# Kernel optimization log

Measured on AMD Instinct MI355X. Metric: run time of the kernel, lower is better.

## Reference

```python
import jax, jax.numpy as jnp
import numpy as np

B, H, W, C_IN, F = 4, 64, 64, 128, 256


def setup_inputs() -> dict:
    key = jax.random.key(0)
    ks = jax.random.split(key, 6)
    return {
        "inputs": jax.random.normal(ks[0], (B, H, W, C_IN), dtype=jnp.float32),
        "W_proj": jax.random.normal(ks[1], (C_IN, F), dtype=jnp.float32) * 0.02,
        "b_proj": jnp.zeros((F,), dtype=jnp.float32),
        "W_q": jax.random.normal(ks[2], (F, F), dtype=jnp.float32) * 0.02,
        "b_q": jnp.zeros((F,), dtype=jnp.float32),
        "W_k": jax.random.normal(ks[3], (F, F), dtype=jnp.float32) * 0.02,
        "b_k": jnp.zeros((F,), dtype=jnp.float32),
        "W_v": jax.random.normal(ks[4], (F, F), dtype=jnp.float32) * 0.02,
        "b_v": jnp.zeros((F,), dtype=jnp.float32),
        "gamma": jax.random.uniform(ks[5], (1,), dtype=jnp.float32),
    }


def reference(inputs, W_proj, b_proj, W_q, b_q, W_k, b_k, W_v, b_v, gamma):
    # 1x1 conv projection (C_in -> filters) since input channels != filters
    x = jnp.einsum("bhwc,cf->bhwf", inputs, W_proj) + b_proj  # [B,H,W,F]
    q = jnp.einsum("bhwf,fg->bhwg", x, W_q) + b_q
    k = jnp.einsum("bhwf,fg->bhwg", x, W_k) + b_k
    v = jnp.einsum("bhwf,fg->bhwg", x, W_v) + b_v
    b, h, w, f = x.shape
    n = h * w
    qr = q.reshape(b, n, f)
    kr = k.reshape(b, n, f)
    vr = v.reshape(b, n, f)
    attn = jax.nn.softmax(jnp.einsum("bnf,bmf->bnm", qr, kr), axis=-1)  # [B,N,N]
    context = jnp.einsum("bnm,bmf->bnf", attn, vr).reshape(b, h, w, f)
    return gamma * context + x
```

## Files before the change

kernel.cpp:

```cpp
#include <hip/hip_runtime.h>
#include <hip/hip_bf16.h>
#include <stdint.h>

typedef __attribute__((ext_vector_type(8))) short short8;
typedef __attribute__((ext_vector_type(4))) float floatx4;
typedef __attribute__((ext_vector_type(16))) float floatx16;
typedef __attribute__((ext_vector_type(2))) long longx2;

#define DEVI __device__ __forceinline__
#define MFMA16(a, b, c) __builtin_amdgcn_mfma_f32_16x16x32_bf16((a), (b), (c), 0, 0, 0)
#define MFMA32(a, b, c) __builtin_amdgcn_mfma_f32_32x32x16_fp8_fp8((a), (b), (c), 0, 0, 0)

typedef __attribute__((address_space(3))) unsigned int lds_u32;
typedef __attribute__((address_space(1))) const unsigned int glb_u32;
#define GLOAD_LDS16(g, l) __builtin_amdgcn_global_load_lds((glb_u32*)(g), (lds_u32*)(l), 16, 0, 0)

DEVI unsigned short f2bf(float x) {
    union { float f; unsigned int u; } v; v.f = x;
    unsigned int r = v.u + 0x7FFFu + ((v.u >> 16) & 1u);
    return (unsigned short)(r >> 16);
}
DEVI float bf2f(unsigned short h) {
    union { unsigned int u; float f; } v; v.u = ((unsigned int)h) << 16;
    return v.f;
}
DEVI unsigned char f2fp8(float x) {
    int c = __builtin_amdgcn_cvt_pk_fp8_f32(x, x, 0, false);
    return (unsigned char)(c & 0xFF);
}

__global__ __launch_bounds__(256) void prep_weights(
    const float* __restrict__ Wp, const float* __restrict__ Wq,
    const float* __restrict__ Wk, const float* __restrict__ Wv,
    unsigned short* __restrict__ Tp, unsigned short* __restrict__ Tq,
    unsigned short* __restrict__ Tk, unsigned short* __restrict__ Tv)
{
    int idx = blockIdx.x * blockDim.x + threadIdx.x;
    if (idx < 32768) {
        int k = idx >> 8, n = idx & 255;
        Tp[n * 128 + k] = f2bf(Wp[idx]);
    } else {
        int r = idx - 32768;
        int m = r >> 16, i = r & 65535;
        const float* W   = (m == 0) ? Wq : (m == 1) ? Wk : Wv;
        unsigned short* T = (m == 0) ? Tq : (m == 1) ? Tk : Tv;
        int k = i >> 8, n = i & 255;
        T[n * 256 + k] = f2bf(W[i]);
    }
}


__global__ __launch_bounds__(256) void gemm_bias(
    const float* __restrict__ A,
    const unsigned short* __restrict__ Wt,
    const float* __restrict__ bias,
    unsigned short* __restrict__ Cb,
    int N)
{
    __shared__ __align__(16) unsigned short As[64][136];
    __shared__ __align__(16) unsigned short Bs[64][136];
    const int tid  = threadIdx.x;
    const int w    = tid >> 6;
    const int lane = tid & 63;
    const int quad = lane >> 4;
    const int l15  = lane & 15;
    const int m0 = blockIdx.x * 64;
    const int n0 = blockIdx.y * 64;

    floatx4 acc[4];
    #pragma unroll
    for (int t = 0; t < 4; ++t) acc[t] = (floatx4)0.0f;

    #pragma unroll
    for (int it = 0; it < 8; ++it) {
        int idx = tid + it * 256;
        int r = idx >> 5, c4 = idx & 31;
        float4 v = *(const float4*)&A[(size_t)(m0 + r) * 128 + c4 * 4];
        ushort4 o;
        o.x = f2bf(v.x); o.y = f2bf(v.y); o.z = f2bf(v.z); o.w = f2bf(v.w);
        *(ushort4*)&As[r][c4 * 4] = o;
    }
    #pragma unroll
    for (int it = 0; it < 4; ++it) {
        int idx = tid + it * 256;
        int r = idx >> 4, g = idx & 15;
        *(short8*)&Bs[r][g * 8] = *(const short8*)&Wt[(size_t)(n0 + r) * 128 + g * 8];
    }
    __syncthreads();
    #pragma unroll
    for (int s = 0; s < 4; ++s) {
        short8 a = *(const short8*)&As[w * 16 + l15][s * 32 + quad * 8];
        #pragma unroll
        for (int t = 0; t < 4; ++t) {
            short8 bfr = *(const short8*)&Bs[t * 16 + l15][s * 32 + quad * 8];
            acc[t] = MFMA16(a, bfr, acc[t]);
        }
    }

    __syncthreads();
    unsigned short* T = &As[0][0];
    #pragma unroll
    for (int t = 0; t < 4; ++t) {
        int n = n0 + t * 16 + l15;
        float bs = bias[n];
        #pragma unroll
        for (int r = 0; r < 4; ++r)
            T[(w * 16 + quad * 4 + r) * 80 + t * 16 + l15] = f2bf(acc[t][r] + bs);
    }
    __syncthreads();
    int row = tid >> 2, c8 = (tid & 3) * 8;
    #pragma unroll
    for (int half = 0; half < 2; ++half) {
        int4 ov = *(const int4*)&T[row * 80 + c8 + half * 32];
        *(int4*)&Cb[(size_t)(m0 + row) * N + n0 + c8 + half * 32] = ov;
    }
}


__global__ __launch_bounds__(256) void gemm_qkv(
    const unsigned short* __restrict__ A,
    const unsigned short* __restrict__ Wt0, const unsigned short* __restrict__ Wt1, const unsigned short* __restrict__ Wt2,
    const float* __restrict__ b0, const float* __restrict__ b1, const float* __restrict__ b2,
    unsigned char* __restrict__ C0, unsigned char* __restrict__ C1, unsigned char* __restrict__ C2,
    int N)
{
    const unsigned short* Wt = (blockIdx.z == 0) ? Wt0 : (blockIdx.z == 1) ? Wt1 : Wt2;
    const float* bias        = (blockIdx.z == 0) ? b0  : (blockIdx.z == 1) ? b1  : b2;
    unsigned char* Cb        = (blockIdx.z == 0) ? C0  : (blockIdx.z == 1) ? C1  : C2;

    __shared__ __align__(16) unsigned short As[64][136];
    __shared__ __align__(16) unsigned short Bs[64][136];
    const int tid  = threadIdx.x;
    const int w    = tid >> 6;
    const int lane = tid & 63;
    const int quad = lane >> 4;
    const int l15  = lane & 15;
    const int m0 = blockIdx.x * 64;
    const int n0 = blockIdx.y * 64;

    floatx4 acc[4];
    #pragma unroll
    for (int t = 0; t < 4; ++t) acc[t] = (floatx4)0.0f;

    for (int kc = 0; kc < 256; kc += 128) {
        __syncthreads();
        #pragma unroll
        for (int idx = tid; idx < 1024; idx += 256) {
            int r = idx >> 4, g = idx & 15;
            *(short8*)&As[r][g * 8] = *(const short8*)&A[(size_t)(m0 + r) * 256 + kc + g * 8];
            *(short8*)&Bs[r][g * 8] = *(const short8*)&Wt[(size_t)(n0 + r) * 256 + kc + g * 8];
        }
        __syncthreads();
        #pragma unroll
        for (int s = 0; s < 4; ++s) {
            short8 a = *(const short8*)&As[w * 16 + l15][s * 32 + quad * 8];
            #pragma unroll
            for (int t = 0; t < 4; ++t) {
                short8 bfr = *(const short8*)&Bs[t * 16 + l15][s * 32 + quad * 8];
                acc[t] = MFMA16(a, bfr, acc[t]);
            }
        }
    }

    __syncthreads();
    unsigned char* T = (unsigned char*)&As[0][0];
    #pragma unroll
    for (int t = 0; t < 4; ++t) {
        int n = n0 + t * 16 + l15;
        float bs = bias[n];
        #pragma unroll
        for (int r = 0; r < 4; ++r)
            T[(w * 16 + quad * 4 + r) * 80 + t * 16 + l15] = f2fp8(acc[t][r] + bs);
    }
    __syncthreads();

    const int b  = m0 >> 12;
    const int mt = (m0 & 4095) >> 5;

    if (blockIdx.z == 0) {
        int row = tid >> 2, c16 = (tid & 3) * 16;
        int4 vq = *(const int4*)&T[row * 80 + c16];
        *(int4*)&Cb[(size_t)(m0 + row) * 256 + n0 + c16] = vq;
    } else {
        const int kt  = tid >> 7;
        const int sub = (tid >> 6) & 1;
        const int ln  = tid & 63;
        const int l31b = ln & 31, hib = ln >> 5;
        union { long h[2]; int4 v; unsigned char bts[16]; } o;
        if (blockIdx.z == 1) {
            #pragma unroll
            for (int h = 0; h < 2; ++h)
                o.h[h] = *(const long*)&T[(kt * 32 + l31b) * 80 + (sub * 2 + h) * 16 + hib * 8];
        } else {
            #pragma unroll
            for (int s2 = 0; s2 < 2; ++s2)
                #pragma unroll
                for (int j = 0; j < 8; ++j)
                    o.bts[s2 * 8 + j] = T[(kt * 32 + s2 * 16 + hib * 8 + j) * 80 + sub * 32 + l31b];
        }
        unsigned char* dst = Cb + (size_t)b * 1048576 + (size_t)(mt + kt) * 8192
                           + (size_t)((n0 >> 5) + sub) * 1024 + ln * 16;
        *(int4*)dst = o.v;
    }
}


__global__ __launch_bounds__(512, 2) void flash_attn(
    const unsigned char* __restrict__ qg,
    const unsigned char* __restrict__ kp,
    const unsigned char* __restrict__ vp,
    const unsigned short* __restrict__ xb,
    const float* __restrict__ gamma,
    float* __restrict__ out)
{
    __shared__ __align__(16) unsigned char KV[2][65536];
    float* MbF = (float*)&KV[0][0];
    float* Ml  = MbF + 64 * 264;

    const int tid  = threadIdx.x;
    const int w    = tid >> 6;
    const int lane = tid & 63;
    const int l31  = lane & 31;
    const int hi   = lane >> 5;
    const int kq   = w & 3;
    const int rw   = w >> 2;
    const int blk  = blockIdx.x;
    const int b    = (blk & 7) >> 1;
    const int rt   = (blk >> 3) * 2 + (blk & 1);
    const int row0 = rt * 64 + rw * 32;

    const size_t baseQ = ((size_t)b * 4096 + row0 + l31) * 256 + hi * 8;
    long qf[16];
    #pragma unroll
    for (int s = 0; s < 16; ++s)
        qf[s] = *(const long*)&qg[baseQ + s * 16];

    const long ones8 = 0x3838383838383838L;

    floatx16 ctx[8];
    #pragma unroll
    for (int i = 0; i < 8; ++i) ctx[i] = (floatx16)0.0f;
    floatx16 lacc = (floatx16)0.0f;

    const unsigned char* kb_b = kp + (size_t)b * 1048576;
    const unsigned char* vb_b = vp + (size_t)b * 1048576;

#define FA_STAGE(T, BUF)                                                             \
    {                                                                                \
        _Pragma("unroll")                                                            \
        for (int p = 0; p < 8; ++p) {                                                \
            const int c    = p * 8 + w;                                              \
            const int ckq  = c >> 4;                                                 \
            const int csel = (c >> 3) & 1;                                           \
            const int coff = (c & 7) * 1024;                                         \
            const unsigned char* src = (csel ? vb_b : kb_b)                          \
                + (size_t)ckq * 262144 + (size_t)(T) * 8192 + coff + lane * 16;      \
            GLOAD_LDS16(src, &KV[BUF][ckq * 16384 + csel * 8192 + coff]);            \
        }                                                                            \
    }

    FA_STAGE(0, 0)

    for (int t = 0; t < 32; ++t) {
        const int buf = t & 1;
        __syncthreads();
        if (t < 31) FA_STAGE(t + 1, buf ^ 1)

        const unsigned char* kc = &KV[buf][kq * 16384];
        const unsigned char* vc = &KV[buf][kq * 16384 + 8192];

        longx2 kk[8];
        #pragma unroll
        for (int p = 0; p < 8; ++p)
            kk[p] = *(const longx2*)&kc[p * 1024 + lane * 16];
        floatx16 sa = (floatx16)0.0f, sb = (floatx16)0.0f;
        __builtin_amdgcn_s_setprio(1);
        #pragma unroll
        for (int p = 0; p < 8; ++p) {
            sa = MFMA32(kk[p].x, qf[2 * p],     sa);
            sb = MFMA32(kk[p].y, qf[2 * p + 1], sb);
        }
        __builtin_amdgcn_s_setprio(0);

        float e[16];
        #pragma unroll
        for (int r = 0; r < 16; ++r) e[r] = __expf(sa[r] + sb[r]);
        int X0 = __builtin_amdgcn_cvt_pk_fp8_f32(e[0],  e[1],  0,  false);
        X0     = __builtin_amdgcn_cvt_pk_fp8_f32(e[2],  e[3],  X0, true);
        int Y0 = __builtin_amdgcn_cvt_pk_fp8_f32(e[4],  e[5],  0,  false);
        Y0     = __builtin_amdgcn_cvt_pk_fp8_f32(e[6],  e[7],  Y0, true);
        int X1 = __builtin_amdgcn_cvt_pk_fp8_f32(e[8],  e[9],  0,  false);
        X1     = __builtin_amdgcn_cvt_pk_fp8_f32(e[10], e[11], X1, true);
        int Y1 = __builtin_amdgcn_cvt_pk_fp8_f32(e[12], e[13], 0,  false);
        Y1     = __builtin_amdgcn_cvt_pk_fp8_f32(e[14], e[15], Y1, true);
        asm volatile("v_permlane32_swap_b32 %0, %1" : "+v"(X0), "+v"(Y0));
        asm volatile("v_permlane32_swap_b32 %0, %1" : "+v"(X1), "+v"(Y1));
        union { int i2[2]; long l; } u0, u1;
        u0.i2[0] = X0; u0.i2[1] = Y0;
        u1.i2[0] = X1; u1.i2[1] = Y1;
        const long ap0 = u0.l;
        const long ap1 = u1.l;

        lacc = MFMA32(ap0, ones8, lacc);
        lacc = MFMA32(ap1, ones8, lacc);
        __builtin_amdgcn_s_setprio(1);
        #pragma unroll
        for (int p = 0; p < 8; ++p) {
            longx2 vv = *(const longx2*)&vc[p * 1024 + lane * 16];
            ctx[p] = MFMA32(ap0, vv.x, ctx[p]);
            ctx[p] = MFMA32(ap1, vv.y, ctx[p]);
        }
        __builtin_amdgcn_s_setprio(0);
    }
#undef FA_STAGE

    __syncthreads();
    for (int pass = 3; pass >= 0; --pass) {
        if (kq == pass) {
            #pragma unroll
            for (int fb = 0; fb < 8; ++fb) {
                #pragma unroll
                for (int r = 0; r < 16; ++r) {
                    int row = rw * 32 + (r & 3) + 8 * (r >> 2) + 4 * hi;
                    int idx = row * 264 + fb * 32 + l31;
                    float prev = (pass == 3) ? 0.0f : MbF[idx];
                    MbF[idx] = prev + ctx[fb][r];
                }
            }
            if (l31 == 0) {
                #pragma unroll
                for (int r = 0; r < 16; ++r) {
                    int row = rw * 32 + (r & 3) + 8 * (r >> 2) + 4 * hi;
                    float prev = (pass == 3) ? 0.0f : Ml[row];
                    Ml[row] = prev + lacc[r];
                }
            }
        }
        __syncthreads();
    }

    const float g = gamma[0];
    const int row = tid >> 3;
    const int c0  = (tid & 7) * 32;
    const float rl = 1.0f / Ml[row];
    const size_t o = ((size_t)b * 4096 + rt * 64 + row) * 256 + c0;
    #pragma unroll
    for (int j = 0; j < 4; ++j) {
        short8 xv = *(const short8*)&xb[o + j * 8];
        float res[8];
        #pragma unroll
        for (int i = 0; i < 8; ++i)
            res[i] = g * MbF[row * 264 + c0 + j * 8 + i] * rl + bf2f((unsigned short)xv[i]);
        *(float4*)&out[o + j * 8]     = *(float4*)&res[0];
        *(float4*)&out[o + j * 8 + 4] = *(float4*)&res[4];
    }
}


extern "C" void kernel_launch(void* const* d_in, const int* in_sizes, int n_in,
                              void* d_out, int out_size, void* d_ws, size_t ws_size,
                              hipStream_t stream)
{
    const float* inp   = (const float*)d_in[0];
    const float* Wp    = (const float*)d_in[1];
    const float* bp    = (const float*)d_in[2];
    const float* Wq    = (const float*)d_in[3];
    const float* bq    = (const float*)d_in[4];
    const float* Wk    = (const float*)d_in[5];
    const float* bk    = (const float*)d_in[6];
    const float* Wv    = (const float*)d_in[7];
    const float* bv    = (const float*)d_in[8];
    const float* gamma = (const float*)d_in[9];
    float* out = (float*)d_out;

    char* ws = (char*)d_ws;
    unsigned char*  q8    = (unsigned char*)(ws + 0);
    unsigned char*  k8    = (unsigned char*)(ws + 4194304);
    unsigned char*  v8    = (unsigned char*)(ws + 8388608);
    unsigned short* x_b   = (unsigned short*)(ws + 12582912);
    unsigned short* Wt_p  = (unsigned short*)(ws + 20971520);
    unsigned short* Wt_q  = (unsigned short*)(ws + 21037056);
    unsigned short* Wt_k  = (unsigned short*)(ws + 21168128);
    unsigned short* Wt_v  = (unsigned short*)(ws + 21299200);

    prep_weights<<<896, 256, 0, stream>>>(Wp, Wq, Wk, Wv, Wt_p, Wt_q, Wt_k, Wt_v);
    gemm_bias<<<dim3(256, 4), 256, 0, stream>>>(inp, Wt_p, bp, x_b, 256);
    gemm_qkv<<<dim3(256, 4, 3), 256, 0, stream>>>(x_b, Wt_q, Wt_k, Wt_v, bq, bk, bv,
                                                  q8, k8, v8, 256);
    flash_attn<<<256, 512, 0, stream>>>(q8, k8, v8, x_b, gamma, out);
}
```

Baseline: 190.4 us.

## Halve attention block tile and stream V from global memory into registers

Shrinks each flash-attention block from 64 to 32 query rows and from 8 to 4 waves, launching twice as many blocks. Only K is staged through LDS now, which halves the LDS buffers and may let more blocks fit per CU. V fragments are loaded straight from global memory into registers, split into two batches placed around the QK MFMA and the softmax so the load latency can overlap compute. In exchange, each V and K tile is no longer shared between two row-waves, so memory traffic roughly doubles. The V reads in the inner loop also take on global-load latency.

```diff
diff --git a/kernel.cpp b/kernel.cpp
--- a/kernel.cpp
+++ b/kernel.cpp
@@ -205,7 +205,7 @@
 }
 
 
-__global__ __launch_bounds__(512, 2) void flash_attn(
+__global__ __launch_bounds__(256, 2) void flash_attn(
     const unsigned char* __restrict__ qg,
     const unsigned char* __restrict__ kp,
     const unsigned char* __restrict__ vp,
@@ -213,21 +213,20 @@
     const float* __restrict__ gamma,
     float* __restrict__ out)
 {
-    __shared__ __align__(16) unsigned char KV[2][65536];
-    float* MbF = (float*)&KV[0][0];
-    float* Ml  = MbF + 64 * 264;
+    __shared__ __align__(16) unsigned char KVb[2][32768];
+    __shared__ float Ml[32];
+    float* MbF = (float*)&KVb[0][0];
 
     const int tid  = threadIdx.x;
     const int w    = tid >> 6;
     const int lane = tid & 63;
     const int l31  = lane & 31;
     const int hi   = lane >> 5;
-    const int kq   = w & 3;
-    const int rw   = w >> 2;
+    const int kq   = w;
     const int blk  = blockIdx.x;
     const int b    = (blk & 7) >> 1;
     const int rt   = (blk >> 3) * 2 + (blk & 1);
-    const int row0 = rt * 64 + rw * 32;
+    const int row0 = rt * 32;
 
     const size_t baseQ = ((size_t)b * 4096 + row0 + l31) * 256 + hi * 8;
     long qf[16];
@@ -243,19 +242,18 @@
     floatx16 lacc = (floatx16)0.0f;
 
     const unsigned char* kb_b = kp + (size_t)b * 1048576;
-    const unsigned char* vb_b = vp + (size_t)b * 1048576;
+    const unsigned char* vq_b = vp + (size_t)b * 1048576 + (size_t)kq * 262144 + lane * 16;
 
 #define FA_STAGE(T, BUF)                                                             \
     {                                                                                \
         _Pragma("unroll")                                                            \
         for (int p = 0; p < 8; ++p) {                                                \
-            const int c    = p * 8 + w;                                              \
-            const int ckq  = c >> 4;                                                 \
-            const int csel = (c >> 3) & 1;                                           \
+            const int c    = p * 4 + w;                                              \
+            const int ckq  = c >> 3;                                                 \
             const int coff = (c & 7) * 1024;                                         \
-            const unsigned char* src = (csel ? vb_b : kb_b)                          \
+            const unsigned char* src = kb_b                                          \
                 + (size_t)ckq * 262144 + (size_t)(T) * 8192 + coff + lane * 16;      \
-            GLOAD_LDS16(src, &KV[BUF][ckq * 16384 + csel * 8192 + coff]);            \
+            GLOAD_LDS16(src, &KVb[BUF][ckq * 8192 + coff]);                          \
         }                                                                            \
     }
 
@@ -266,8 +264,12 @@
         __syncthreads();
         if (t < 31) FA_STAGE(t + 1, buf ^ 1)
 
-        const unsigned char* kc = &KV[buf][kq * 16384];
-        const unsigned char* vc = &KV[buf][kq * 16384 + 8192];
+        const unsigned char* kc = &KVb[buf][kq * 8192];
+        const unsigned char* vt = vq_b + (size_t)t * 8192;
+
+        longx2 v0[4];
+        #pragma unroll
+        for (int p = 0; p < 4; ++p) v0[p] = *(const longx2*)&vt[p * 1024];
 
         longx2 kk[8];
         #pragma unroll
@@ -281,6 +283,10 @@
             sb = MFMA32(kk[p].y, qf[2 * p + 1], sb);
         }
         __builtin_amdgcn_s_setprio(0);
+
+        longx2 v1[4];
+        #pragma unroll
+        for (int p = 0; p < 4; ++p) v1[p] = *(const longx2*)&vt[(4 + p) * 1024];
 
         float e[16];
         #pragma unroll
@@ -305,10 +311,14 @@
         lacc = MFMA32(ap1, ones8, lacc);
         __builtin_amdgcn_s_setprio(1);
         #pragma unroll
-        for (int p = 0; p < 8; ++p) {
-            longx2 vv = *(const longx2*)&vc[p * 1024 + lane * 16];
-            ctx[p] = MFMA32(ap0, vv.x, ctx[p]);
-            ctx[p] = MFMA32(ap1, vv.y, ctx[p]);
+        for (int p = 0; p < 4; ++p) {
+            ctx[p] = MFMA32(ap0, v0[p].x, ctx[p]);
+            ctx[p] = MFMA32(ap1, v0[p].y, ctx[p]);
+        }
+        #pragma unroll
+        for (int p = 0; p < 4; ++p) {
+            ctx[4 + p] = MFMA32(ap0, v1[p].x, ctx[4 + p]);
+            ctx[4 + p] = MFMA32(ap1, v1[p].y, ctx[4 + p]);
         }
         __builtin_amdgcn_s_setprio(0);
     }
@@ -321,7 +331,7 @@
             for (int fb = 0; fb < 8; ++fb) {
                 #pragma unroll
                 for (int r = 0; r < 16; ++r) {
-                    int row = rw * 32 + (r & 3) + 8 * (r >> 2) + 4 * hi;
+                    int row = (r & 3) + 8 * (r >> 2) + 4 * hi;
                     int idx = row * 264 + fb * 32 + l31;
                     float prev = (pass == 3) ? 0.0f : MbF[idx];
                     MbF[idx] = prev + ctx[fb][r];
@@ -330,7 +340,7 @@
             if (l31 == 0) {
                 #pragma unroll
                 for (int r = 0; r < 16; ++r) {
-                    int row = rw * 32 + (r & 3) + 8 * (r >> 2) + 4 * hi;
+                    int row = (r & 3) + 8 * (r >> 2) + 4 * hi;
                     float prev = (pass == 3) ? 0.0f : Ml[row];
                     Ml[row] = prev + lacc[r];
                 }
@@ -343,7 +353,7 @@
     const int row = tid >> 3;
     const int c0  = (tid & 7) * 32;
     const float rl = 1.0f / Ml[row];
-    const size_t o = ((size_t)b * 4096 + rt * 64 + row) * 256 + c0;
+    const size_t o = ((size_t)b * 4096 + rt * 32 + row) * 256 + c0;
     #pragma unroll
     for (int j = 0; j < 4; ++j) {
         short8 xv = *(const short8*)&xb[o + j * 8];
@@ -387,5 +397,5 @@
     gemm_bias<<<dim3(256, 4), 256, 0, stream>>>(inp, Wt_p, bp, x_b, 256);
     gemm_qkv<<<dim3(256, 4, 3), 256, 0, stream>>>(x_b, Wt_q, Wt_k, Wt_v, bq, bk, bv,
                                                   q8, k8, v8, 256);
-    flash_attn<<<256, 512, 0, stream>>>(q8, k8, v8, x_b, gamma, out);
-}
+    flash_attn<<<512, 256, 0, stream>>>(q8, k8, v8, x_b, gamma, out);
+}
```

Measured after the change: 238.8 us. 25.4% more time.

## Tile weight transpose through LDS and reuse A tile across all N in QKV GEMM

Applied to the files above, without the earlier changes.

The weight prep kernel now transposes each 64x64 tile through shared memory, so global reads use float4 and global writes are 16-byte coalesced instead of scattered 2-byte stores. The QKV GEMM loads the full 64x256 A tile once per block and loops over all four N tiles internally, which removes the redundant A reloads across blockIdx.y. The cost is a grid reduced from 3072 to 768 blocks and much more LDS per block (~72KB), which lowers occupancy and leaves less parallelism to hide latency.

```diff
diff --git a/kernel.cpp b/kernel.cpp
--- a/kernel.cpp
+++ b/kernel.cpp
@@ -35,17 +35,33 @@
     unsigned short* __restrict__ Tp, unsigned short* __restrict__ Tq,
     unsigned short* __restrict__ Tk, unsigned short* __restrict__ Tv)
 {
-    int idx = blockIdx.x * blockDim.x + threadIdx.x;
-    if (idx < 32768) {
-        int k = idx >> 8, n = idx & 255;
-        Tp[n * 128 + k] = f2bf(Wp[idx]);
-    } else {
-        int r = idx - 32768;
-        int m = r >> 16, i = r & 65535;
-        const float* W   = (m == 0) ? Wq : (m == 1) ? Wk : Wv;
-        unsigned short* T = (m == 0) ? Tq : (m == 1) ? Tk : Tv;
-        int k = i >> 8, n = i & 255;
-        T[n * 256 + k] = f2bf(W[i]);
+    __shared__ unsigned short Tl[64][72];
+    const int bb = blockIdx.x;
+    const float* W; unsigned short* T; int K; int tt;
+    if (bb < 8)       { W = Wp; T = Tp; K = 128; tt = bb;      }
+    else if (bb < 24) { W = Wq; T = Tq; K = 256; tt = bb - 8;  }
+    else if (bb < 40) { W = Wk; T = Tk; K = 256; tt = bb - 24; }
+    else              { W = Wv; T = Tv; K = 256; tt = bb - 40; }
+    const int r0 = (tt >> 2) * 64;
+    const int c0 = (tt & 3) * 64;
+    const int tid = threadIdx.x;
+
+    #pragma unroll
+    for (int i = 0; i < 4; ++i) {
+        int u = tid + i * 256;
+        int r = u >> 4, c4 = u & 15;
+        float4 v = *(const float4*)&W[(size_t)(r0 + r) * 256 + c0 + c4 * 4];
+        Tl[c4 * 4 + 0][r] = f2bf(v.x);
+        Tl[c4 * 4 + 1][r] = f2bf(v.y);
+        Tl[c4 * 4 + 2][r] = f2bf(v.z);
+        Tl[c4 * 4 + 3][r] = f2bf(v.w);
+    }
+    __syncthreads();
+    #pragma unroll
+    for (int i = 0; i < 2; ++i) {
+        int u = tid + i * 256;
+        int orow = u >> 3, g = u & 7;
+        *(short8*)&T[(size_t)(c0 + orow) * K + r0 + g * 8] = *(const short8*)&Tl[orow][g * 8];
     }
 }
 
@@ -128,31 +144,41 @@
     const float* bias        = (blockIdx.z == 0) ? b0  : (blockIdx.z == 1) ? b1  : b2;
     unsigned char* Cb        = (blockIdx.z == 0) ? C0  : (blockIdx.z == 1) ? C1  : C2;
 
-    __shared__ __align__(16) unsigned short As[64][136];
-    __shared__ __align__(16) unsigned short Bs[64][136];
+    __shared__ __align__(16) unsigned short As[64][264];
+    __shared__ __align__(16) unsigned short Bs[64][264];
+    __shared__ __align__(16) unsigned char  Tt[64 * 80];
     const int tid  = threadIdx.x;
     const int w    = tid >> 6;
     const int lane = tid & 63;
     const int quad = lane >> 4;
     const int l15  = lane & 15;
     const int m0 = blockIdx.x * 64;
-    const int n0 = blockIdx.y * 64;
-
-    floatx4 acc[4];
-    #pragma unroll
-    for (int t = 0; t < 4; ++t) acc[t] = (floatx4)0.0f;
-
-    for (int kc = 0; kc < 256; kc += 128) {
+
+    #pragma unroll
+    for (int it = 0; it < 8; ++it) {
+        int u = tid + it * 256;
+        int r = u >> 5, g = u & 31;
+        *(short8*)&As[r][g * 8] = *(const short8*)&A[(size_t)(m0 + r) * 256 + g * 8];
+    }
+
+    const int b  = m0 >> 12;
+    const int mt = (m0 & 4095) >> 5;
+
+    for (int nt = 0; nt < 4; ++nt) {
         __syncthreads();
         #pragma unroll
-        for (int idx = tid; idx < 1024; idx += 256) {
-            int r = idx >> 4, g = idx & 15;
-            *(short8*)&As[r][g * 8] = *(const short8*)&A[(size_t)(m0 + r) * 256 + kc + g * 8];
-            *(short8*)&Bs[r][g * 8] = *(const short8*)&Wt[(size_t)(n0 + r) * 256 + kc + g * 8];
+        for (int it = 0; it < 8; ++it) {
+            int u = tid + it * 256;
+            int r = u >> 5, g = u & 31;
+            *(short8*)&Bs[r][g * 8] = *(const short8*)&Wt[(size_t)(nt * 64 + r) * 256 + g * 8];
         }
         __syncthreads();
-        #pragma unroll
-        for (int s = 0; s < 4; ++s) {
+
+        floatx4 acc[4];
+        #pragma unroll
+        for (int t = 0; t < 4; ++t) acc[t] = (floatx4)0.0f;
+        #pragma unroll
+        for (int s = 0; s < 8; ++s) {
             short8 a = *(const short8*)&As[w * 16 + l15][s * 32 + quad * 8];
             #pragma unroll
             for (int t = 0; t < 4; ++t) {
@@ -160,47 +186,43 @@
                 acc[t] = MFMA16(a, bfr, acc[t]);
             }
         }
-    }
-
-    __syncthreads();
-    unsigned char* T = (unsigned char*)&As[0][0];
-    #pragma unroll
-    for (int t = 0; t < 4; ++t) {
-        int n = n0 + t * 16 + l15;
-        float bs = bias[n];
-        #pragma unroll
-        for (int r = 0; r < 4; ++r)
-            T[(w * 16 + quad * 4 + r) * 80 + t * 16 + l15] = f2fp8(acc[t][r] + bs);
-    }
-    __syncthreads();
-
-    const int b  = m0 >> 12;
-    const int mt = (m0 & 4095) >> 5;
-
-    if (blockIdx.z == 0) {
-        int row = tid >> 2, c16 = (tid & 3) * 16;
-        int4 vq = *(const int4*)&T[row * 80 + c16];
-        *(int4*)&Cb[(size_t)(m0 + row) * 256 + n0 + c16] = vq;
-    } else {
-        const int kt  = tid >> 7;
-        const int sub = (tid >> 6) & 1;
-        const int ln  = tid & 63;
-        const int l31b = ln & 31, hib = ln >> 5;
-        union { long h[2]; int4 v; unsigned char bts[16]; } o;
-        if (blockIdx.z == 1) {
+
+        const int n0 = nt * 64;
+        #pragma unroll
+        for (int t = 0; t < 4; ++t) {
+            int n = n0 + t * 16 + l15;
+            float bs = bias[n];
             #pragma unroll
-            for (int h = 0; h < 2; ++h)
-                o.h[h] = *(const long*)&T[(kt * 32 + l31b) * 80 + (sub * 2 + h) * 16 + hib * 8];
+            for (int r = 0; r < 4; ++r)
+                Tt[(w * 16 + quad * 4 + r) * 80 + t * 16 + l15] = f2fp8(acc[t][r] + bs);
+        }
+        __syncthreads();
+
+        if (blockIdx.z == 0) {
+            int row = tid >> 2, c16 = (tid & 3) * 16;
+            int4 vq = *(const int4*)&Tt[row * 80 + c16];
+            *(int4*)&Cb[(size_t)(m0 + row) * 256 + n0 + c16] = vq;
         } else {
-            #pragma unroll
-            for (int s2 = 0; s2 < 2; ++s2)
+            const int kt  = tid >> 7;
+            const int sub = (tid >> 6) & 1;
+            const int ln  = tid & 63;
+            const int l31b = ln & 31, hib = ln >> 5;
+            union { long h[2]; int4 v; unsigned char bts[16]; } o;
+            if (blockIdx.z == 1) {
                 #pragma unroll
-                for (int j = 0; j < 8; ++j)
-                    o.bts[s2 * 8 + j] = T[(kt * 32 + s2 * 16 + hib * 8 + j) * 80 + sub * 32 + l31b];
-        }
-        unsigned char* dst = Cb + (size_t)b * 1048576 + (size_t)(mt + kt) * 8192
-                           + (size_t)((n0 >> 5) + sub) * 1024 + ln * 16;
-        *(int4*)dst = o.v;
+                for (int h = 0; h < 2; ++h)
+                    o.h[h] = *(const long*)&Tt[(kt * 32 + l31b) * 80 + (sub * 2 + h) * 16 + hib * 8];
+            } else {
+                #pragma unroll
+                for (int s2 = 0; s2 < 2; ++s2)
+                    #pragma unroll
+                    for (int j = 0; j < 8; ++j)
+                        o.bts[s2 * 8 + j] = Tt[(kt * 32 + s2 * 16 + hib * 8 + j) * 80 + sub * 32 + l31b];
+            }
+            unsigned char* dst = Cb + (size_t)b * 1048576 + (size_t)(mt + kt) * 8192
+                               + (size_t)((n0 >> 5) + sub) * 1024 + ln * 16;
+            *(int4*)dst = o.v;
+        }
     }
 }
 
@@ -383,9 +405,9 @@
     unsigned short* Wt_k  = (unsigned short*)(ws + 21168128);
     unsigned short* Wt_v  = (unsigned short*)(ws + 21299200);
 
-    prep_weights<<<896, 256, 0, stream>>>(Wp, Wq, Wk, Wv, Wt_p, Wt_q, Wt_k, Wt_v);
+    prep_weights<<<56, 256, 0, stream>>>(Wp, Wq, Wk, Wv, Wt_p, Wt_q, Wt_k, Wt_v);
     gemm_bias<<<dim3(256, 4), 256, 0, stream>>>(inp, Wt_p, bp, x_b, 256);
-    gemm_qkv<<<dim3(256, 4, 3), 256, 0, stream>>>(x_b, Wt_q, Wt_k, Wt_v, bq, bk, bv,
+    gemm_qkv<<<dim3(256, 1, 3), 256, 0, stream>>>(x_b, Wt_q, Wt_k, Wt_v, bq, bk, bv,
                                                   q8, k8, v8, 256);
     flash_attn<<<256, 512, 0, stream>>>(q8, k8, v8, x_b, gamma, out);
 }
```

New measurement: 187.8 us, median of 2. No clear change (-1.4%).
